# Kernel tuning notes

Hardware: AMD Instinct MI355X
Metric: run time of the kernel (lower is better)

Reference implementation:

```python
import jax, jax.numpy as jnp
import numpy as np


def _rot_grids(group_order, ks, dtype):
    """Normalized sampling grids for each rotation (align_corners=False convention)."""
    k = jnp.arange(group_order, dtype=dtype)
    theta = 2.0 * jnp.pi * k / group_order                      # [G]
    c, s = jnp.cos(theta), jnp.sin(theta)
    # F.affine_grid base coords with align_corners=False: centers of pixels in [-1,1]
    lin = (jnp.arange(ks, dtype=dtype) + 0.5) * (2.0 / ks) - 1.0
    y, x = jnp.meshgrid(lin, lin, indexing='ij')                 # [ks,ks] each
    # theta rows: [cos, -sin, 0], [sin, cos, 0] applied to (x, y, 1)
    gx = c[:, None, None] * x - s[:, None, None] * y             # [G,ks,ks]
    gy = s[:, None, None] * x + c[:, None, None] * y             # [G,ks,ks]
    return gx, gy


def _grid_sample_bilinear_zeros(img, gx, gy):
    """Bilinear grid_sample, padding_mode='zeros', align_corners=False.
    img: [C,H,W]; gx,gy: [G,H,W] normalized coords. Returns [C,G,H,W]."""
    C, H, W = img.shape
    dt = img.dtype
    # unnormalize (align_corners=False)
    ix = ((gx + 1.0) * W - 1.0) * 0.5
    iy = ((gy + 1.0) * H - 1.0) * 0.5
    ix0 = jnp.floor(ix)
    iy0 = jnp.floor(iy)
    wx1 = (ix - ix0).astype(dt); wx0 = 1.0 - wx1
    wy1 = (iy - iy0).astype(dt); wy0 = 1.0 - wy1

    def gather(iyf, ixf):
        xi = ixf.astype(jnp.int32)
        yi = iyf.astype(jnp.int32)
        valid = ((xi >= 0) & (xi < W) & (yi >= 0) & (yi < H)).astype(dt)
        xi_c = jnp.clip(xi, 0, W - 1)
        yi_c = jnp.clip(yi, 0, H - 1)
        return img[:, yi_c, xi_c] * valid                        # [C,G,H,W]

    out = (gather(iy0, ix0) * (wy0 * wx0)
           + gather(iy0, ix0 + 1.0) * (wy0 * wx1)
           + gather(iy0 + 1.0, ix0) * (wy1 * wx0)
           + gather(iy0 + 1.0, ix0 + 1.0) * (wy1 * wx1))
    return out


def setup_inputs() -> dict:
    key = jax.random.key(0)
    out_ch, in_ch, ks = 512, 256, 9
    base_weight = jax.random.normal(key, (out_ch, in_ch, ks, ks), dtype=jnp.float32)
    return {"base_weight": base_weight, "group_order": 8}


def reference(base_weight, group_order):
    O, I, ks, _ = base_weight.shape
    img = base_weight.reshape(O * I, ks, ks)                     # [C,H,W]
    gx, gy = _rot_grids(group_order, ks, base_weight.dtype)      # [G,ks,ks]
    out = _grid_sample_bilinear_zeros(img, gx, gy)               # [C,G,ks,ks]
    # concat over rotations along dim 0 -> [G*O, I, ks, ks]
    out = out.reshape(O, I, group_order, ks, ks).transpose(2, 0, 1, 3, 4)
    return out.reshape(group_order * O, I, ks, ks)
```

## Files before the change

### kernel.cpp

```cpp
#include <hip/hip_runtime.h>
#include <math.h>


#define KS   9
#define NPIX 81
#define NC   128
#define BLOCK 256

__global__ void st_make_table(float* __restrict__ tab, int G) {
    int i = blockIdx.x * blockDim.x + threadIdx.x;
    if (i >= G * NPIX) return;
    int g = i / NPIX;
    int p = i - g * NPIX;
    int py = p / KS, px = p - py * KS;
    double theta = 6.283185307179586 * (double)g / (double)G;
    double cth = cos(theta), sth = sin(theta);
    double lx = ((double)px + 0.5) * (2.0 / KS) - 1.0;
    double ly = ((double)py + 0.5) * (2.0 / KS) - 1.0;
    double gx = cth * lx - sth * ly;
    double gy = sth * lx + cth * ly;
    double ix = ((gx + 1.0) * KS - 1.0) * 0.5;
    double iy = ((gy + 1.0) * KS - 1.0) * 0.5;
    double ix0 = floor(ix), iy0 = floor(iy);
    double fx = ix - ix0, fy = iy - iy0;
    int xi0 = (int)ix0, yi0 = (int)iy0;
    float w[4]; int o[4];
#pragma unroll
    for (int k = 0; k < 4; ++k) {
        int dx = k & 1, dy = k >> 1;
        int xi = xi0 + dx, yi = yi0 + dy;
        bool valid = (xi >= 0) && (xi < KS) && (yi >= 0) && (yi < KS);
        double wv = (dy ? fy : 1.0 - fy) * (dx ? fx : 1.0 - fx);
        int xc = xi < 0 ? 0 : (xi > KS - 1 ? KS - 1 : xi);
        int yc = yi < 0 ? 0 : (yi > KS - 1 ? KS - 1 : yi);
        w[k] = valid ? (float)wv : 0.0f;
        o[k] = (yc * KS + xc) * 4;
    }
    float4* e0 = (float4*)(tab + (size_t)i * 8);
    *e0 = make_float4(w[0], w[1], w[2], w[3]);
    int4* e1 = (int4*)(tab + (size_t)i * 8 + 4);
    *e1 = make_int4(o[0], o[1], o[2], o[3]);
}

__global__ __launch_bounds__(BLOCK) void st_rotate(
        const float* __restrict__ in, const float* __restrict__ tab,
        float* __restrict__ out, int C, int G) {
    __shared__ __align__(16) float lin[NC * NPIX];
    const int t = threadIdx.x;
    const int c0 = blockIdx.x * NC;

    {
        const float4* src = (const float4*)(in + (size_t)c0 * NPIX);
        float4* dst = (float4*)lin;
        for (int j = t; j < NC * NPIX / 4; j += BLOCK) dst[j] = src[j];
    }
    __syncthreads();

    if (t < 3 * NPIX) {
        const int c_local = t / NPIX;
        const int p = t - c_local * NPIX;
        const float4* tab4 = (const float4*)tab;
        for (int g = 0; g < G; ++g) {
            const float4 w = tab4[(size_t)(g * NPIX + p) * 2];
            const int4  o = ((const int4*)tab4)[(size_t)(g * NPIX + p) * 2 + 1];
            float* og = out + ((size_t)g * C + c0) * NPIX + t;
            const char* lb = (const char*)lin + c_local * (NPIX * 4);
            for (int cc = 0; cc < NC; cc += 3) {
                if (cc + c_local < NC) {
                    float v = *(const float*)(lb + o.x) * w.x
                            + *(const float*)(lb + o.y) * w.y
                            + *(const float*)(lb + o.z) * w.z
                            + *(const float*)(lb + o.w) * w.w;
                    *og = v;
                }
                lb += 3 * NPIX * 4;
                og += 3 * NPIX;
            }
        }
    }
}

extern "C" void kernel_launch(void* const* d_in, const int* in_sizes, int n_in,
                              void* d_out, int out_size, void* d_ws, size_t ws_size,
                              hipStream_t stream) {
    const float* in = (const float*)d_in[0];
    float* out = (float*)d_out;
    float* tab = (float*)d_ws;
    const int C = in_sizes[0] / NPIX;
    const int G = out_size / in_sizes[0];
    const int ents = G * NPIX;
    st_make_table<<<(ents + 255) / 256, 256, 0, stream>>>(tab, G);
    st_rotate<<<C / NC, BLOCK, 0, stream>>>(in, tab, out, C, G);
}
```

Measured before the change: 385.1 us.

## Halve channel tile, pack bilinear table as row pairs, specialize and unroll loops

Cuts the channel tile from 128 to 64 so each block uses less LDS and more blocks run per CU. The lookup table is reorganised into one float4 of weights plus two row base offsets, where each row reads two adjacent LDS entries; clamping the base x index keeps both taps in range. The rotation count is made a template parameter for the common G=8 case, and the channel loop is fully unrolled with a fixed trip count. Together these aim to raise occupancy, shrink table traffic and cut loop and address overhead, in exchange for more registers and code that hard-codes NC=64 with three channels per thread.

```diff
diff --git a/kernel.cpp b/kernel.cpp
--- a/kernel.cpp
+++ b/kernel.cpp
@@ -4,78 +4,86 @@
 
 #define KS   9
 #define NPIX 81
-#define NC   128
+#define NC   64
 #define BLOCK 256
+#define NENT_MAX 648
 
-__global__ void st_make_table(float* __restrict__ tab, int G) {
+__global__ void st_make_table(float4* __restrict__ tw, int2* __restrict__ tb, int G) {
     int i = blockIdx.x * blockDim.x + threadIdx.x;
     if (i >= G * NPIX) return;
-    int g = i / NPIX;
-    int p = i - g * NPIX;
+    int g = i / NPIX, p = i - g * NPIX;
     int py = p / KS, px = p - py * KS;
-    double theta = 6.283185307179586 * (double)g / (double)G;
-    double cth = cos(theta), sth = sin(theta);
+    double th = 6.283185307179586 * (double)g / (double)G;
+    double ct = cos(th), st = sin(th);
     double lx = ((double)px + 0.5) * (2.0 / KS) - 1.0;
     double ly = ((double)py + 0.5) * (2.0 / KS) - 1.0;
-    double gx = cth * lx - sth * ly;
-    double gy = sth * lx + cth * ly;
+    double gx = ct * lx - st * ly;
+    double gy = st * lx + ct * ly;
     double ix = ((gx + 1.0) * KS - 1.0) * 0.5;
     double iy = ((gy + 1.0) * KS - 1.0) * 0.5;
-    double ix0 = floor(ix), iy0 = floor(iy);
-    double fx = ix - ix0, fy = iy - iy0;
-    int xi0 = (int)ix0, yi0 = (int)iy0;
-    float w[4]; int o[4];
+    double fx = ix - floor(ix), fy = iy - floor(iy);
+    int xi0 = (int)floor(ix), yi0 = (int)floor(iy);
+    int xb = xi0 < 0 ? 0 : (xi0 > KS - 2 ? KS - 2 : xi0);
+    double wa = (xi0 >= 0 && xi0 < KS) ? (1.0 - fx) : 0.0;
+    double wb = (xi0 + 1 >= 0 && xi0 + 1 < KS) ? fx : 0.0;
+    double w0 = (xi0 == xb ? wa : 0.0) + (xi0 + 1 == xb ? wb : 0.0);
+    double w1 = (xi0 == xb + 1 ? wa : 0.0) + (xi0 + 1 == xb + 1 ? wb : 0.0);
+    float W[2][2]; int B[2];
 #pragma unroll
-    for (int k = 0; k < 4; ++k) {
-        int dx = k & 1, dy = k >> 1;
-        int xi = xi0 + dx, yi = yi0 + dy;
-        bool valid = (xi >= 0) && (xi < KS) && (yi >= 0) && (yi < KS);
-        double wv = (dy ? fy : 1.0 - fy) * (dx ? fx : 1.0 - fx);
-        int xc = xi < 0 ? 0 : (xi > KS - 1 ? KS - 1 : xi);
-        int yc = yi < 0 ? 0 : (yi > KS - 1 ? KS - 1 : yi);
-        w[k] = valid ? (float)wv : 0.0f;
-        o[k] = (yc * KS + xc) * 4;
+    for (int r = 0; r < 2; ++r) {
+        int y = yi0 + r;
+        double wy = (r ? fy : 1.0 - fy) * ((y >= 0 && y < KS) ? 1.0 : 0.0);
+        int yc = y < 0 ? 0 : (y > KS - 1 ? KS - 1 : y);
+        W[r][0] = (float)(wy * w0);
+        W[r][1] = (float)(wy * w1);
+        B[r] = yc * KS + xb;
     }
-    float4* e0 = (float4*)(tab + (size_t)i * 8);
-    *e0 = make_float4(w[0], w[1], w[2], w[3]);
-    int4* e1 = (int4*)(tab + (size_t)i * 8 + 4);
-    *e1 = make_int4(o[0], o[1], o[2], o[3]);
+    tw[i] = make_float4(W[0][0], W[0][1], W[1][0], W[1][1]);
+    tb[i] = make_int2(B[0], B[1]);
 }
 
+template <int GO>
 __global__ __launch_bounds__(BLOCK) void st_rotate(
-        const float* __restrict__ in, const float* __restrict__ tab,
-        float* __restrict__ out, int C, int G) {
-    __shared__ __align__(16) float lin[NC * NPIX];
+        const float* __restrict__ in, const float4* __restrict__ tw,
+        const int2* __restrict__ tb, float* __restrict__ out, int C, int Grt) {
+    __shared__ float lin[NC * NPIX];
     const int t = threadIdx.x;
     const int c0 = blockIdx.x * NC;
 
     {
         const float4* src = (const float4*)(in + (size_t)c0 * NPIX);
         float4* dst = (float4*)lin;
-        for (int j = t; j < NC * NPIX / 4; j += BLOCK) dst[j] = src[j];
+#pragma unroll
+        for (int j = 0; j < (NC * NPIX / 4 + BLOCK - 1) / BLOCK; ++j) {
+            int idx = j * BLOCK + t;
+            if (idx < NC * NPIX / 4) dst[idx] = src[idx];
+        }
     }
     __syncthreads();
 
-    if (t < 3 * NPIX) {
-        const int c_local = t / NPIX;
-        const int p = t - c_local * NPIX;
-        const float4* tab4 = (const float4*)tab;
-        for (int g = 0; g < G; ++g) {
-            const float4 w = tab4[(size_t)(g * NPIX + p) * 2];
-            const int4  o = ((const int4*)tab4)[(size_t)(g * NPIX + p) * 2 + 1];
-            float* og = out + ((size_t)g * C + c0) * NPIX + t;
-            const char* lb = (const char*)lin + c_local * (NPIX * 4);
-            for (int cc = 0; cc < NC; cc += 3) {
-                if (cc + c_local < NC) {
-                    float v = *(const float*)(lb + o.x) * w.x
-                            + *(const float*)(lb + o.y) * w.y
-                            + *(const float*)(lb + o.z) * w.z
-                            + *(const float*)(lb + o.w) * w.w;
-                    *og = v;
-                }
-                lb += 3 * NPIX * 4;
-                og += 3 * NPIX;
-            }
+    if (t >= 3 * NPIX) return;
+    const int c_local = t / NPIX;
+    const int p = t - c_local * NPIX;
+    const int G = GO > 0 ? GO : Grt;
+
+#pragma unroll
+    for (int g = 0; g < G; ++g) {
+        const float4 w = tw[g * NPIX + p];
+        const int2  b = tb[g * NPIX + p];
+        const int i0 = c_local * NPIX + b.x;
+        const int i1 = c_local * NPIX + b.y;
+        float* og = out + ((size_t)g * C + c0) * NPIX + t;
+#pragma unroll
+        for (int cc = 0; cc < 21; ++cc) {
+            const int cb = cc * (3 * NPIX);
+            float v = lin[cb + i0] * w.x + lin[cb + i0 + 1] * w.y
+                    + lin[cb + i1] * w.z + lin[cb + i1 + 1] * w.w;
+            og[cc * (3 * NPIX)] = v;
+        }
+        if (c_local == 0) {
+            const int cb = 21 * (3 * NPIX);
+            og[cb] = lin[cb + i0] * w.x + lin[cb + i0 + 1] * w.y
+                   + lin[cb + i1] * w.z + lin[cb + i1 + 1] * w.w;
         }
     }
 }
@@ -85,10 +93,14 @@
                               hipStream_t stream) {
     const float* in = (const float*)d_in[0];
     float* out = (float*)d_out;
-    float* tab = (float*)d_ws;
     const int C = in_sizes[0] / NPIX;
     const int G = out_size / in_sizes[0];
+    float4* tw = (float4*)d_ws;
+    int2*   tb = (int2*)((char*)d_ws + NENT_MAX * 16);
     const int ents = G * NPIX;
-    st_make_table<<<(ents + 255) / 256, 256, 0, stream>>>(tab, G);
-    st_rotate<<<C / NC, BLOCK, 0, stream>>>(in, tab, out, C, G);
+    st_make_table<<<(ents + 255) / 256, 256, 0, stream>>>(tw, tb, G);
+    if (G == 8)
+        st_rotate<8><<<C / NC, BLOCK, 0, stream>>>(in, tw, tb, out, C, G);
+    else
+        st_rotate<0><<<C / NC, BLOCK, 0, stream>>>(in, tw, tb, out, C, G);
 }
```

Result: no change. 388.7 us (+0.9%).
